# Performance work log

Measured on AMD Instinct MI355X. Metric: run time of the kernel, lower is better.

## Reference

```python
import jax, jax.numpy as jnp
import numpy as np

N, E, F, H, A, C, NC, L, AH = 50000, 800000, 768, 256, 128, 128, 7, 2, 4

def _ln(x, g, b):
    m = jnp.mean(x, axis=-1, keepdims=True)
    v = jnp.var(x, axis=-1, keepdims=True)
    return (x - m) / jnp.sqrt(v + 1e-5) * g + b

def setup_inputs() -> dict:
    key = jax.random.key(0)
    ks = jax.random.split(key, 32)
    s = 0.02
    d = {}
    d['x'] = jax.random.normal(ks[0], (N, F), jnp.float32)
    d['edge_index'] = jax.random.randint(ks[1], (2, E), 0, N, jnp.int32)
    d['W_in'] = jax.random.normal(ks[2], (F, H), jnp.float32) * s
    d['b_in'] = jnp.zeros((H,), jnp.float32)
    d['gin_W1'] = jax.random.normal(ks[3], (L, H, H), jnp.float32) * s
    d['gin_b1'] = jnp.zeros((L, H), jnp.float32)
    d['gin_lng'] = jnp.ones((L, H), jnp.float32)
    d['gin_lnb'] = jnp.zeros((L, H), jnp.float32)
    d['gin_W2'] = jax.random.normal(ks[4], (L, H, H), jnp.float32) * s
    d['gin_b2'] = jnp.zeros((L, H), jnp.float32)
    d['eps'] = jnp.zeros((L,), jnp.float32)
    d['ln_g'] = jnp.ones((L, H), jnp.float32)
    d['ln_b'] = jnp.zeros((L, H), jnp.float32)
    d['att_W1'] = jax.random.normal(ks[5], (AH, H, A), jnp.float32) * s
    d['att_b1'] = jnp.zeros((AH, A), jnp.float32)
    d['att_W2'] = jax.random.normal(ks[6], (AH, A), jnp.float32) * s
    d['att_b2'] = jnp.zeros((AH,), jnp.float32)
    d['Wc1'] = jax.random.normal(ks[7], (H, C), jnp.float32) * s
    d['bc1'] = jnp.zeros((C,), jnp.float32)
    d['lnc1_g'] = jnp.ones((C,), jnp.float32)
    d['lnc1_b'] = jnp.zeros((C,), jnp.float32)
    d['Wc2'] = jax.random.normal(ks[8], (C, C // 2), jnp.float32) * s
    d['bc2'] = jnp.zeros((C // 2,), jnp.float32)
    d['lnc2_g'] = jnp.ones((C // 2,), jnp.float32)
    d['lnc2_b'] = jnp.zeros((C // 2,), jnp.float32)
    d['Wc3'] = jax.random.normal(ks[9], (C // 2, NC), jnp.float32) * s
    d['bc3'] = jnp.zeros((NC,), jnp.float32)
    return d

def reference(x, edge_index, W_in, b_in, gin_W1, gin_b1, gin_lng, gin_lnb, gin_W2, gin_b2, eps, ln_g, ln_b, att_W1, att_b1, att_W2, att_b2, Wc1, bc1, lnc1_g, lnc1_b, Wc2, bc2, lnc2_g, lnc2_b, Wc3, bc3):
    src, dst = edge_index[0], edge_index[1]
    # input projection (use_residual and input_dim != gnn_hidden)
    h = x @ W_in + b_in  # [N,H]
    for i in range(L):
        agg = jax.ops.segment_sum(h[src], dst, num_segments=N)  # GIN sum aggregation
        m = (1.0 + eps[i]) * h + agg
        m = _ln(m @ gin_W1[i] + gin_b1[i], gin_lng[i], gin_lnb[i])
        m = jax.nn.relu(m) @ gin_W2[i] + gin_b2[i]
        hn = jax.nn.relu(_ln(m, ln_g[i], ln_b[i]))
        h = hn + h  # residual (shapes match)
    # multi-head attention pooling, softmax over node dim
    s = jnp.tanh(jnp.einsum('nd,kda->kna', h, att_W1) + att_b1[:, None, :])  # [AH,N,A]
    logits = jnp.einsum('kna,ka->kn', s, att_W2) + att_b2[:, None]  # [AH,N]
    a = jax.nn.softmax(logits, axis=1)  # [AH,N]
    z = jnp.einsum('kn,nd->kd', a, h)  # [AH,H]
    z_agg = jnp.mean(z, axis=0)  # [H]
    attn = a.T  # [N,AH]
    # classifier (full variant)
    c = jax.nn.relu(_ln(z_agg @ Wc1 + bc1, lnc1_g, lnc1_b))
    c = jax.nn.relu(_ln(c @ Wc2 + bc2, lnc2_g, lnc2_b))
    probs = jax.nn.softmax(c @ Wc3 + bc3, axis=0)
    return probs, attn
```

## Files before the change

### kernel.cpp

```cpp
#include <hip/hip_runtime.h>
#include <math.h>

#define NN 50000
#define NE 800000
#define FF 768
#define HH 256

typedef __attribute__((ext_vector_type(8))) short short8;
typedef __attribute__((ext_vector_type(4))) float f32x4;

__device__ inline unsigned short f2bf(float f) {
  unsigned u = __float_as_uint(f);
  u = u + 0x7fffu + ((u >> 16) & 1u);
  return (unsigned short)(u >> 16);
}
__device__ inline float bf2f(unsigned short b) {
  return __uint_as_float(((unsigned)b) << 16);
}

__device__ __forceinline__ void ldsload16(const unsigned short* g, unsigned short* l) {
  __builtin_amdgcn_global_load_lds(
      (const __attribute__((address_space(1))) void*)g,
      (__attribute__((address_space(3))) void*)l, 16, 0, 0);
}

__global__ void k_count(const int* __restrict__ dstv, int* __restrict__ deg) {
  int e = blockIdx.x * 256 + threadIdx.x;
  if (e < NE) atomicAdd(&deg[dstv[e]], 1);
}

__global__ void k_scan(const int* __restrict__ deg, int* __restrict__ rowptr) {
  const int CH = 49;
  int tid = threadIdx.x;
  int lane = tid & 63, w = tid >> 6;
  int base = tid * CH;
  int sum = 0;
  for (int i = 0; i < CH; i++) {
    int idx = base + i;
    if (idx < NN) sum += deg[idx];
  }
  int incl = sum;
  for (int off = 1; off < 64; off <<= 1) {
    int tv = __shfl_up(incl, off, 64);
    if (lane >= off) incl += tv;
  }
  __shared__ int ws[16];
  if (lane == 63) ws[w] = incl;
  __syncthreads();
  if (tid == 0) {
    int c = 0;
    for (int i = 0; i < 16; i++) { int tv = ws[i]; ws[i] = c; c += tv; }
  }
  __syncthreads();
  int run = ws[w] + (incl - sum);
  if (tid == 0) rowptr[0] = 0;
  for (int i = 0; i < CH; i++) {
    int idx = base + i;
    if (idx < NN) { run += deg[idx]; rowptr[idx + 1] = run; }
  }
}

__global__ void k_scatter(const int* __restrict__ srcv, const int* __restrict__ dstv,
                          int* __restrict__ cursor, int* __restrict__ csr_src) {
  int e = blockIdx.x * 256 + threadIdx.x;
  if (e < NE) {
    int d = dstv[e];
    int pos = atomicAdd(&cursor[d], 1);
    csr_src[pos] = srcv[e];
  }
}

__global__ void k_agg(const unsigned short* __restrict__ hb, const int* __restrict__ rowptr,
                      const int* __restrict__ csr_src, const float* __restrict__ eps,
                      int layer, unsigned short* __restrict__ mb) {
  int node = (blockIdx.x * blockDim.x + threadIdx.x) >> 6;
  int lane = threadIdx.x & 63;
  if (node >= NN) return;
  int beg = rowptr[node], end = rowptr[node + 1];
  const ushort4* hv = (const ushort4*)hb;
  float ax = 0.f, ay = 0.f, az = 0.f, aw = 0.f;
  for (int e = beg; e < end; ++e) {
    int s = csr_src[e];
    ushort4 v = hv[(size_t)s * 64 + lane];
    ax += bf2f(v.x); ay += bf2f(v.y); az += bf2f(v.z); aw += bf2f(v.w);
  }
  float ep = 1.0f + eps[layer];
  ushort4 h0 = hv[(size_t)node * 64 + lane];
  ax += ep * bf2f(h0.x); ay += ep * bf2f(h0.y);
  az += ep * bf2f(h0.z); aw += ep * bf2f(h0.w);
  ushort4 o;
  o.x = f2bf(ax); o.y = f2bf(ay); o.z = f2bf(az); o.w = f2bf(aw);
  *(ushort4*)&mb[(size_t)node * 256 + lane * 4] = o;
}

__global__ void k_tcast(const float* __restrict__ src0, unsigned short* __restrict__ dst0,
                        int R, int C) {
  const float* src = src0 + (size_t)blockIdx.z * R * C;
  unsigned short* dst = dst0 + (size_t)blockIdx.z * R * C;
  __shared__ float tile[32][33];
  int bx = blockIdx.x * 32, by = blockIdx.y * 32;
  int tx = threadIdx.x & 31, ty = threadIdx.x >> 5;
  for (int i = 0; i < 32; i += 8) {
    int r = by + ty + i, c = bx + tx;
    tile[ty + i][tx] = (r < R && c < C) ? src[(size_t)r * C + c] : 0.f;
  }
  __syncthreads();
  for (int i = 0; i < 32; i += 8) {
    int c = bx + ty + i, r = by + tx;
    if (c < C && r < R) dst[(size_t)c * R + r] = f2bf(tile[tx][ty + i]);
  }
}

template <int KTOT, int EPI, bool AF32, bool WF>
__global__ __launch_bounds__(256) void k_mm(
    const void* __restrict__ Ap, const unsigned short* __restrict__ Bt,
    const float* __restrict__ bias, const float* __restrict__ g,
    const float* __restrict__ be, const float* __restrict__ resid,
    float* __restrict__ outf, unsigned short* __restrict__ outb) {
  __shared__ unsigned short As[64 * 32];
  __shared__ unsigned short Bs[256 * 32];
  __shared__ float redS[4][64];
  __shared__ float redQ[4][64];
  __shared__ float mvM[64], mvI[64];
  int t = threadIdx.x, lane = t & 63, wave = t >> 6;
  int row0 = blockIdx.x * 64;
  f32x4 acc[4][4];
#pragma unroll
  for (int i = 0; i < 4; i++)
#pragma unroll
    for (int j = 0; j < 4; j++) acc[i][j] = (f32x4)(0.f);
  int m16 = lane & 15, kq = lane >> 4;

  int arow = t >> 2, a2 = t & 3;
  int asl = a2 ^ (arow & 3);
  int agr = row0 + arow; if (agr >= NN) agr = NN - 1;
  unsigned short* AsDst = &As[wave * 512];
  int brow_[4], bsl_[4];
#pragma unroll
  for (int j = 0; j < 4; j++) {
    int s = j * 256 + t;
    brow_[j] = s >> 2;
    bsl_[j] = (s & 3) ^ (brow_[j] & 3);
  }

  for (int k0 = 0; k0 < KTOT; k0 += 32) {
    if (AF32) {
      const float* Af = (const float*)Ap + (size_t)agr * KTOT + k0 + asl * 8;
      float4 f0 = *(const float4*)Af;
      float4 f1 = *(const float4*)(Af + 4);
      short8 v;
      v[0] = (short)f2bf(f0.x); v[1] = (short)f2bf(f0.y);
      v[2] = (short)f2bf(f0.z); v[3] = (short)f2bf(f0.w);
      v[4] = (short)f2bf(f1.x); v[5] = (short)f2bf(f1.y);
      v[6] = (short)f2bf(f1.z); v[7] = (short)f2bf(f1.w);
      *(short8*)&As[arow * 32 + a2 * 8] = v;
    } else {
      ldsload16((const unsigned short*)Ap + (size_t)agr * KTOT + k0 + asl * 8, AsDst);
    }
#pragma unroll
    for (int j = 0; j < 4; j++)
      ldsload16(&Bt[(size_t)brow_[j] * KTOT + k0 + bsl_[j] * 8],
                &Bs[(j * 256 + wave * 64) * 8]);
    __syncthreads();
    short8 a[4], b[4];
#pragma unroll
    for (int rt = 0; rt < 4; rt++) {
      int row = rt * 16 + m16;
      a[rt] = *(const short8*)&As[row * 32 + ((kq ^ (row & 3)) * 8)];
    }
#pragma unroll
    for (int ct = 0; ct < 4; ct++) {
      int row = wave * 64 + ct * 16 + m16;
      b[ct] = *(const short8*)&Bs[row * 32 + ((kq ^ (row & 3)) * 8)];
    }
#pragma unroll
    for (int rt = 0; rt < 4; rt++)
#pragma unroll
      for (int ct = 0; ct < 4; ct++)
        acc[rt][ct] = __builtin_amdgcn_mfma_f32_16x16x32_bf16(a[rt], b[ct], acc[rt][ct], 0, 0, 0);
    __syncthreads();
  }

  int colbase = wave * 64 + m16;
  float bv[4];
#pragma unroll
  for (int ct = 0; ct < 4; ct++) bv[ct] = bias[colbase + ct * 16];

  if (EPI == 0) {
#pragma unroll
    for (int rt = 0; rt < 4; rt++)
#pragma unroll
      for (int reg = 0; reg < 4; reg++) {
        int r = row0 + rt * 16 + kq * 4 + reg;
        if (r < NN) {
#pragma unroll
          for (int ct = 0; ct < 4; ct++) {
            float v = acc[rt][ct][reg] + bv[ct];
            outf[(size_t)r * 256 + colbase + ct * 16] = v;
            outb[(size_t)r * 256 + colbase + ct * 16] = f2bf(v);
          }
        }
      }
    return;
  }

  float s[4][4], q[4][4];
#pragma unroll
  for (int rt = 0; rt < 4; rt++)
#pragma unroll
    for (int reg = 0; reg < 4; reg++) { s[rt][reg] = 0.f; q[rt][reg] = 0.f; }
#pragma unroll
  for (int rt = 0; rt < 4; rt++)
#pragma unroll
    for (int ct = 0; ct < 4; ct++)
#pragma unroll
      for (int reg = 0; reg < 4; reg++) {
        float v = acc[rt][ct][reg] + bv[ct];
        acc[rt][ct][reg] = v;
        s[rt][reg] += v;
        q[rt][reg] += v * v;
      }
#pragma unroll
  for (int off = 1; off < 16; off <<= 1) {
#pragma unroll
    for (int rt = 0; rt < 4; rt++)
#pragma unroll
      for (int reg = 0; reg < 4; reg++) {
        s[rt][reg] += __shfl_xor(s[rt][reg], off, 64);
        q[rt][reg] += __shfl_xor(q[rt][reg], off, 64);
      }
  }
  if (m16 == 0) {
#pragma unroll
    for (int rt = 0; rt < 4; rt++)
#pragma unroll
      for (int reg = 0; reg < 4; reg++) {
        redS[wave][rt * 16 + kq * 4 + reg] = s[rt][reg];
        redQ[wave][rt * 16 + kq * 4 + reg] = q[rt][reg];
      }
  }
  __syncthreads();
  if (t < 64) {
    float ss = redS[0][t] + redS[1][t] + redS[2][t] + redS[3][t];
    float qq = redQ[0][t] + redQ[1][t] + redQ[2][t] + redQ[3][t];
    float mean = ss * (1.f / 256.f);
    float var = qq * (1.f / 256.f) - mean * mean;
    mvM[t] = mean;
    mvI[t] = rsqrtf(var + 1e-5f);
  }
  __syncthreads();
  float gv[4], bev[4];
#pragma unroll
  for (int ct = 0; ct < 4; ct++) { gv[ct] = g[colbase + ct * 16]; bev[ct] = be[colbase + ct * 16]; }
#pragma unroll
  for (int rt = 0; rt < 4; rt++)
#pragma unroll
    for (int reg = 0; reg < 4; reg++) {
      int rr = rt * 16 + kq * 4 + reg;
      int r = row0 + rr;
      if (r >= NN) continue;
      float mean = mvM[rr], inv = mvI[rr];
#pragma unroll
      for (int ct = 0; ct < 4; ct++) {
        int col = colbase + ct * 16;
        float val = fmaxf((acc[rt][ct][reg] - mean) * inv * gv[ct] + bev[ct], 0.f);
        if (EPI == 2) {
          val += resid[(size_t)r * 256 + col];
          if (WF) outf[(size_t)r * 256 + col] = val;
        }
        outb[(size_t)r * 256 + col] = f2bf(val);
      }
    }
}

__global__ __launch_bounds__(256) void k_att(const unsigned short* __restrict__ hb,
    const unsigned short* __restrict__ W1T, const float* __restrict__ b1,
    const float* __restrict__ W2, const float* __restrict__ b2,
    float* __restrict__ logitsT) {
  __shared__ unsigned short As[64 * 32];
  __shared__ unsigned short Bs[512 * 32];
  int t = threadIdx.x, lane = t & 63, wave = t >> 6;
  int row0 = blockIdx.x * 64;
  f32x4 acc[4][8];
#pragma unroll
  for (int i = 0; i < 4; i++)
#pragma unroll
    for (int j = 0; j < 8; j++) acc[i][j] = (f32x4)(0.f);
  int m16 = lane & 15, kq = lane >> 4;
  int arow = t >> 2, a2 = t & 3;
  int asl = a2 ^ (arow & 3);
  int agr = row0 + arow; if (agr >= NN) agr = NN - 1;
  unsigned short* AsDst = &As[wave * 512];
  int brow_[8], bsl_[8];
#pragma unroll
  for (int j = 0; j < 8; j++) {
    int s = j * 256 + t;
    brow_[j] = s >> 2;
    bsl_[j] = (s & 3) ^ (brow_[j] & 3);
  }
  for (int k0 = 0; k0 < 256; k0 += 32) {
    ldsload16(&hb[(size_t)agr * 256 + k0 + asl * 8], AsDst);
#pragma unroll
    for (int j = 0; j < 8; j++)
      ldsload16(&W1T[(size_t)brow_[j] * 256 + k0 + bsl_[j] * 8],
                &Bs[(j * 256 + wave * 64) * 8]);
    __syncthreads();
    short8 a[4];
#pragma unroll
    for (int rt = 0; rt < 4; rt++) {
      int row = rt * 16 + m16;
      a[rt] = *(const short8*)&As[row * 32 + ((kq ^ (row & 3)) * 8)];
    }
#pragma unroll
    for (int ct = 0; ct < 8; ct++) {
      int row = wave * 128 + ct * 16 + m16;
      short8 b = *(const short8*)&Bs[row * 32 + ((kq ^ (row & 3)) * 8)];
#pragma unroll
      for (int rt = 0; rt < 4; rt++)
        acc[rt][ct] = __builtin_amdgcn_mfma_f32_16x16x32_bf16(a[rt], b, acc[rt][ct], 0, 0, 0);
    }
    __syncthreads();
  }
  const float* b1k = b1 + wave * 128;
  const float* w2k = W2 + wave * 128;
  float p[4][4];
#pragma unroll
  for (int rt = 0; rt < 4; rt++)
#pragma unroll
    for (int reg = 0; reg < 4; reg++) p[rt][reg] = 0.f;
#pragma unroll
  for (int ct = 0; ct < 8; ct++) {
    int col = ct * 16 + m16;
    float b1v = b1k[col], w2v = w2k[col];
#pragma unroll
    for (int rt = 0; rt < 4; rt++)
#pragma unroll
      for (int reg = 0; reg < 4; reg++) {
        float xv = acc[rt][ct][reg] + b1v;
        xv = fminf(fmaxf(xv, -10.f), 10.f);
        float ex = __expf(2.f * xv);
        p[rt][reg] += (ex - 1.f) / (ex + 1.f) * w2v;
      }
  }
#pragma unroll
  for (int off = 1; off < 16; off <<= 1)
#pragma unroll
    for (int rt = 0; rt < 4; rt++)
#pragma unroll
      for (int reg = 0; reg < 4; reg++) p[rt][reg] += __shfl_xor(p[rt][reg], off, 64);
  if (m16 == 0) {
    float b2v = b2[wave];
#pragma unroll
    for (int rt = 0; rt < 4; rt++)
#pragma unroll
      for (int reg = 0; reg < 4; reg++) {
        int r = row0 + rt * 16 + kq * 4 + reg;
        if (r < NN) logitsT[(size_t)wave * NN + r] = p[rt][reg] + b2v;
      }
  }
}

__global__ void k_smax1(const float* __restrict__ logitsT, float* __restrict__ pmax,
                        float* __restrict__ psum) {
  int k = blockIdx.y;
  int tid = threadIdx.x;
  const float* L = logitsT + (size_t)k * NN;
  __shared__ float sm[256];
  float mx = -1e30f;
  for (int i = blockIdx.x * 256 + tid; i < NN; i += 128 * 256) mx = fmaxf(mx, L[i]);
  sm[tid] = mx; __syncthreads();
  for (int o = 128; o >= 1; o >>= 1) { if (tid < o) sm[tid] = fmaxf(sm[tid], sm[tid + o]); __syncthreads(); }
  float bmax = sm[0];
  __syncthreads();
  float s = 0.f;
  for (int i = blockIdx.x * 256 + tid; i < NN; i += 128 * 256) s += __expf(L[i] - bmax);
  sm[tid] = s; __syncthreads();
  for (int o = 128; o >= 1; o >>= 1) { if (tid < o) sm[tid] += sm[tid + o]; __syncthreads(); }
  if (tid == 0) { pmax[k * 128 + blockIdx.x] = bmax; psum[k * 128 + blockIdx.x] = sm[0]; }
}

__global__ void k_smax2(const float* __restrict__ pmax, const float* __restrict__ psum,
                        float* __restrict__ gs) {
  int k = blockIdx.x;
  int tid = threadIdx.x;
  __shared__ float sm[128], sv[128];
  float m = pmax[k * 128 + tid];
  sm[tid] = m; __syncthreads();
  for (int o = 64; o >= 1; o >>= 1) { if (tid < o) sm[tid] = fmaxf(sm[tid], sm[tid + o]); __syncthreads(); }
  float gm = sm[0];
  __syncthreads();
  sv[tid] = psum[k * 128 + tid] * __expf(m - gm);
  __syncthreads();
  for (int o = 64; o >= 1; o >>= 1) { if (tid < o) sv[tid] += sv[tid + o]; __syncthreads(); }
  if (tid == 0) { gs[k * 2] = gm; gs[k * 2 + 1] = sv[0]; }
}

__global__ void k_attnz(const float* __restrict__ logitsT, const float* __restrict__ gs,
                        const unsigned short* __restrict__ hb, float* __restrict__ out_attn,
                        float* __restrict__ z) {
  int n0 = blockIdx.x * 128;
  int tid = threadIdx.x;
  __shared__ float a[4][128];
  for (int i = tid; i < 512; i += 256) {
    int k = i >> 7, n = i & 127;
    float v = 0.f;
    if (n0 + n < NN) v = __expf(logitsT[(size_t)k * NN + n0 + n] - gs[k * 2]) / gs[k * 2 + 1];
    a[k][n] = v;
  }
  __syncthreads();
  for (int i = tid; i < 512; i += 256) {
    int n = i >> 2, k = i & 3;
    if (n0 + n < NN) out_attn[(size_t)(n0 + n) * 4 + k] = a[k][n];
  }
  float z0 = 0.f, z1 = 0.f, z2 = 0.f, z3 = 0.f;
  int d = tid;
  int nmax = NN - n0; if (nmax > 128) nmax = 128;
  for (int n = 0; n < nmax; n++) {
    float hv = bf2f(hb[(size_t)(n0 + n) * 256 + d]);
    z0 += a[0][n] * hv; z1 += a[1][n] * hv; z2 += a[2][n] * hv; z3 += a[3][n] * hv;
  }
  atomicAdd(&z[0 * 256 + d], z0);
  atomicAdd(&z[1 * 256 + d], z1);
  atomicAdd(&z[2 * 256 + d], z2);
  atomicAdd(&z[3 * 256 + d], z3);
}

__global__ void k_cls(const float* __restrict__ z, const float* __restrict__ Wc1,
                      const float* __restrict__ bc1, const float* __restrict__ g1,
                      const float* __restrict__ b1, const float* __restrict__ Wc2,
                      const float* __restrict__ bc2, const float* __restrict__ g2,
                      const float* __restrict__ b2, const float* __restrict__ Wc3,
                      const float* __restrict__ bc3, float* __restrict__ out) {
  int tid = threadIdx.x;
  __shared__ float za[256];
  __shared__ float buf[256];
  __shared__ float c1s[128];
  __shared__ float c2s[64];
  za[tid] = 0.25f * (z[tid] + z[256 + tid] + z[512 + tid] + z[768 + tid]);
  __syncthreads();
  float v1 = 0.f;
  if (tid < 128) {
    for (int d = 0; d < 256; d++) v1 += za[d] * Wc1[d * 128 + tid];
    v1 += bc1[tid];
  }
  buf[tid] = (tid < 128) ? v1 : 0.f; __syncthreads();
  for (int o = 128; o >= 1; o >>= 1) { if (tid < o) buf[tid] += buf[tid + o]; __syncthreads(); }
  float mean1 = buf[0] * (1.f / 128.f);
  __syncthreads();
  buf[tid] = (tid < 128) ? (v1 - mean1) * (v1 - mean1) : 0.f; __syncthreads();
  for (int o = 128; o >= 1; o >>= 1) { if (tid < o) buf[tid] += buf[tid + o]; __syncthreads(); }
  float inv1 = rsqrtf(buf[0] * (1.f / 128.f) + 1e-5f);
  __syncthreads();
  if (tid < 128) c1s[tid] = fmaxf((v1 - mean1) * inv1 * g1[tid] + b1[tid], 0.f);
  __syncthreads();
  float v2 = 0.f;
  if (tid < 64) {
    for (int d = 0; d < 128; d++) v2 += c1s[d] * Wc2[d * 64 + tid];
    v2 += bc2[tid];
  }
  buf[tid] = (tid < 64) ? v2 : 0.f; __syncthreads();
  for (int o = 128; o >= 1; o >>= 1) { if (tid < o) buf[tid] += buf[tid + o]; __syncthreads(); }
  float mean2 = buf[0] * (1.f / 64.f);
  __syncthreads();
  buf[tid] = (tid < 64) ? (v2 - mean2) * (v2 - mean2) : 0.f; __syncthreads();
  for (int o = 128; o >= 1; o >>= 1) { if (tid < o) buf[tid] += buf[tid + o]; __syncthreads(); }
  float inv2 = rsqrtf(buf[0] * (1.f / 64.f) + 1e-5f);
  __syncthreads();
  if (tid < 64) c2s[tid] = fmaxf((v2 - mean2) * inv2 * g2[tid] + b2[tid], 0.f);
  __syncthreads();
  if (tid < 7) {
    float l = 0.f;
    for (int d = 0; d < 64; d++) l += c2s[d] * Wc3[d * 7 + tid];
    buf[tid] = l + bc3[tid];
  }
  __syncthreads();
  if (tid == 0) {
    float mx = -1e30f;
    for (int i = 0; i < 7; i++) mx = fmaxf(mx, buf[i]);
    float s = 0.f;
    for (int i = 0; i < 7; i++) s += __expf(buf[i] - mx);
    for (int i = 0; i < 7; i++) out[i] = __expf(buf[i] - mx) / s;
  }
}

extern "C" void kernel_launch(void* const* d_in, const int* in_sizes, int n_in,
                              void* d_out, int out_size, void* d_ws, size_t ws_size,
                              hipStream_t stream) {
  const float* x       = (const float*)d_in[0];
  const int*   ei      = (const int*)d_in[1];
  const float* W_in    = (const float*)d_in[2];
  const float* b_in    = (const float*)d_in[3];
  const float* gin_W1  = (const float*)d_in[4];
  const float* gin_b1  = (const float*)d_in[5];
  const float* gin_lng = (const float*)d_in[6];
  const float* gin_lnb = (const float*)d_in[7];
  const float* gin_W2  = (const float*)d_in[8];
  const float* gin_b2  = (const float*)d_in[9];
  const float* eps     = (const float*)d_in[10];
  const float* ln_g    = (const float*)d_in[11];
  const float* ln_b    = (const float*)d_in[12];
  const float* att_W1  = (const float*)d_in[13];
  const float* att_b1  = (const float*)d_in[14];
  const float* att_W2  = (const float*)d_in[15];
  const float* att_b2  = (const float*)d_in[16];
  const float* Wc1     = (const float*)d_in[17];
  const float* bc1     = (const float*)d_in[18];
  const float* lnc1_g  = (const float*)d_in[19];
  const float* lnc1_b  = (const float*)d_in[20];
  const float* Wc2     = (const float*)d_in[21];
  const float* bc2     = (const float*)d_in[22];
  const float* lnc2_g  = (const float*)d_in[23];
  const float* lnc2_b  = (const float*)d_in[24];
  const float* Wc3     = (const float*)d_in[25];
  const float* bc3     = (const float*)d_in[26];
  float* out = (float*)d_out;
  (void)in_sizes; (void)n_in; (void)out_size; (void)ws_size;

  char* wsb = (char*)d_ws;
  size_t off = 0;
  auto alloc = [&](size_t bytes) {
    char* p = wsb + off;
    off += (bytes + 255) & ~(size_t)255;
    return p;
  };
  float*          h       = (float*)alloc((size_t)NN * HH * 4);
  unsigned short* hb      = (unsigned short*)alloc((size_t)NN * HH * 2);
  unsigned short* mb1     = (unsigned short*)alloc((size_t)NN * HH * 2);
  unsigned short* mb2     = (unsigned short*)alloc((size_t)NN * HH * 2);
  unsigned short* WinT    = (unsigned short*)alloc((size_t)HH * FF * 2);
  unsigned short* g1T     = (unsigned short*)alloc((size_t)2 * HH * HH * 2);
  unsigned short* g2T     = (unsigned short*)alloc((size_t)2 * HH * HH * 2);
  unsigned short* aW1T    = (unsigned short*)alloc((size_t)4 * 128 * HH * 2);
  float*          logitsT = (float*)alloc((size_t)4 * NN * 4);
  int*            deg     = (int*)alloc((size_t)NN * 4);
  int*            rowptr  = (int*)alloc((size_t)(NN + 1) * 4);
  int*            cursor  = (int*)alloc((size_t)NN * 4);
  int*            csr_src = (int*)alloc((size_t)NE * 4);
  float*          pmax    = (float*)alloc(4 * 128 * 4);
  float*          psum    = (float*)alloc(4 * 128 * 4);
  float*          gs      = (float*)alloc(8 * 4);
  float*          z       = (float*)alloc(4 * 256 * 4);

  const int* srcv = ei;
  const int* dstv = ei + NE;

  k_tcast<<<dim3((HH + 31) / 32, (FF + 31) / 32, 1), 256, 0, stream>>>(W_in, WinT, FF, HH);
  k_tcast<<<dim3(8, 8, 2), 256, 0, stream>>>(gin_W1, g1T, HH, HH);
  k_tcast<<<dim3(8, 8, 2), 256, 0, stream>>>(gin_W2, g2T, HH, HH);
  k_tcast<<<dim3(4, 8, 4), 256, 0, stream>>>(att_W1, aW1T, HH, 128);

  hipMemsetAsync(deg, 0, (size_t)NN * 4, stream);
  hipMemsetAsync(z, 0, 4 * 256 * 4, stream);
  k_count<<<(NE + 255) / 256, 256, 0, stream>>>(dstv, deg);
  k_scan<<<1, 1024, 0, stream>>>(deg, rowptr);
  hipMemcpyAsync(cursor, rowptr, (size_t)NN * 4, hipMemcpyDeviceToDevice, stream);
  k_scatter<<<(NE + 255) / 256, 256, 0, stream>>>(srcv, dstv, cursor, csr_src);

  int gblocks = (NN + 63) / 64;
  k_mm<FF, 0, true, true><<<gblocks, 256, 0, stream>>>(x, WinT, b_in, nullptr, nullptr, nullptr, h, hb);

  for (int l = 0; l < 2; l++) {
    k_agg<<<(NN + 3) / 4, 256, 0, stream>>>(hb, rowptr, csr_src, eps, l, mb1);
    k_mm<HH, 1, false, true><<<gblocks, 256, 0, stream>>>(mb1, g1T + (size_t)l * HH * HH,
        gin_b1 + l * HH, gin_lng + l * HH, gin_lnb + l * HH, nullptr, nullptr, mb2);
    if (l == 0)
      k_mm<HH, 2, false, true><<<gblocks, 256, 0, stream>>>(mb2, g2T + (size_t)l * HH * HH,
          gin_b2 + l * HH, ln_g + l * HH, ln_b + l * HH, h, h, hb);
    else
      k_mm<HH, 2, false, false><<<gblocks, 256, 0, stream>>>(mb2, g2T + (size_t)l * HH * HH,
          gin_b2 + l * HH, ln_g + l * HH, ln_b + l * HH, h, nullptr, hb);
  }

  k_att<<<gblocks, 256, 0, stream>>>(hb, aW1T, att_b1, att_W2, att_b2, logitsT);
  k_smax1<<<dim3(128, 4), 256, 0, stream>>>(logitsT, pmax, psum);
  k_smax2<<<4, 128, 0, stream>>>(pmax, psum, gs);
  k_attnz<<<(NN + 127) / 128, 256, 0, stream>>>(logitsT, gs, hb, out + 7, z);
  k_cls<<<1, 256, 0, stream>>>(z, Wc1, bc1, lnc1_g, lnc1_b, Wc2, bc2, lnc2_g, lnc2_b,
                               Wc3, bc3, out);
}
```

Baseline: 935.2 us.

## Double-buffer LDS loads in bf16 GIN matmuls with explicit waitcnt pipelining

Splits the templated matmul into a float-input projection kernel and a bf16-input hidden kernel. The hidden kernel double-buffers the A and B tiles in LDS, prefetching two K-chunks ahead with global_load_lds and using s_waitcnt vmcnt plus raw barriers so loads overlap the MFMA work. The goal is to hide global memory latency in the four 256-wide GIN matmuls. In exchange it doubles LDS use per block, which may lower occupancy, and it depends on hand-counted vmcnt values being correct.

```diff
diff --git a/kernel.cpp b/kernel.cpp
--- a/kernel.cpp
+++ b/kernel.cpp
@@ -111,17 +111,12 @@
   }
 }
 
-template <int KTOT, int EPI, bool AF32, bool WF>
-__global__ __launch_bounds__(256) void k_mm(
-    const void* __restrict__ Ap, const unsigned short* __restrict__ Bt,
-    const float* __restrict__ bias, const float* __restrict__ g,
-    const float* __restrict__ be, const float* __restrict__ resid,
-    float* __restrict__ outf, unsigned short* __restrict__ outb) {
+__global__ __launch_bounds__(256) void k_mmff(
+    const float* __restrict__ x, const unsigned short* __restrict__ Bt,
+    const float* __restrict__ bias, float* __restrict__ outf,
+    unsigned short* __restrict__ outb) {
   __shared__ unsigned short As[64 * 32];
   __shared__ unsigned short Bs[256 * 32];
-  __shared__ float redS[4][64];
-  __shared__ float redQ[4][64];
-  __shared__ float mvM[64], mvI[64];
   int t = threadIdx.x, lane = t & 63, wave = t >> 6;
   int row0 = blockIdx.x * 64;
   f32x4 acc[4][4];
@@ -130,11 +125,9 @@
 #pragma unroll
     for (int j = 0; j < 4; j++) acc[i][j] = (f32x4)(0.f);
   int m16 = lane & 15, kq = lane >> 4;
-
   int arow = t >> 2, a2 = t & 3;
   int asl = a2 ^ (arow & 3);
   int agr = row0 + arow; if (agr >= NN) agr = NN - 1;
-  unsigned short* AsDst = &As[wave * 512];
   int brow_[4], bsl_[4];
 #pragma unroll
   for (int j = 0; j < 4; j++) {
@@ -142,10 +135,9 @@
     brow_[j] = s >> 2;
     bsl_[j] = (s & 3) ^ (brow_[j] & 3);
   }
-
-  for (int k0 = 0; k0 < KTOT; k0 += 32) {
-    if (AF32) {
-      const float* Af = (const float*)Ap + (size_t)agr * KTOT + k0 + asl * 8;
+  for (int k0 = 0; k0 < FF; k0 += 32) {
+    {
+      const float* Af = x + (size_t)agr * FF + k0 + asl * 8;
       float4 f0 = *(const float4*)Af;
       float4 f1 = *(const float4*)(Af + 4);
       short8 v;
@@ -154,12 +146,10 @@
       v[4] = (short)f2bf(f1.x); v[5] = (short)f2bf(f1.y);
       v[6] = (short)f2bf(f1.z); v[7] = (short)f2bf(f1.w);
       *(short8*)&As[arow * 32 + a2 * 8] = v;
-    } else {
-      ldsload16((const unsigned short*)Ap + (size_t)agr * KTOT + k0 + asl * 8, AsDst);
     }
 #pragma unroll
     for (int j = 0; j < 4; j++)
-      ldsload16(&Bt[(size_t)brow_[j] * KTOT + k0 + bsl_[j] * 8],
+      ldsload16(&Bt[(size_t)brow_[j] * FF + k0 + bsl_[j] * 8],
                 &Bs[(j * 256 + wave * 64) * 8]);
     __syncthreads();
     short8 a[4], b[4];
@@ -180,29 +170,102 @@
         acc[rt][ct] = __builtin_amdgcn_mfma_f32_16x16x32_bf16(a[rt], b[ct], acc[rt][ct], 0, 0, 0);
     __syncthreads();
   }
-
   int colbase = wave * 64 + m16;
   float bv[4];
 #pragma unroll
   for (int ct = 0; ct < 4; ct++) bv[ct] = bias[colbase + ct * 16];
-
-  if (EPI == 0) {
-#pragma unroll
-    for (int rt = 0; rt < 4; rt++)
-#pragma unroll
-      for (int reg = 0; reg < 4; reg++) {
-        int r = row0 + rt * 16 + kq * 4 + reg;
-        if (r < NN) {
-#pragma unroll
-          for (int ct = 0; ct < 4; ct++) {
-            float v = acc[rt][ct][reg] + bv[ct];
-            outf[(size_t)r * 256 + colbase + ct * 16] = v;
-            outb[(size_t)r * 256 + colbase + ct * 16] = f2bf(v);
-          }
+#pragma unroll
+  for (int rt = 0; rt < 4; rt++)
+#pragma unroll
+    for (int reg = 0; reg < 4; reg++) {
+      int r = row0 + rt * 16 + kq * 4 + reg;
+      if (r < NN) {
+#pragma unroll
+        for (int ct = 0; ct < 4; ct++) {
+          float v = acc[rt][ct][reg] + bv[ct];
+          outf[(size_t)r * 256 + colbase + ct * 16] = v;
+          outb[(size_t)r * 256 + colbase + ct * 16] = f2bf(v);
         }
       }
-    return;
-  }
+    }
+}
+
+template <int EPI, bool WF>
+__global__ __launch_bounds__(256) void k_mmh(
+    const unsigned short* __restrict__ Ab, const unsigned short* __restrict__ Bt,
+    const float* __restrict__ bias, const float* __restrict__ g,
+    const float* __restrict__ be, const float* __restrict__ resid,
+    float* __restrict__ outf, unsigned short* __restrict__ outb) {
+  __shared__ unsigned short As[2][64 * 32];
+  __shared__ unsigned short Bs[2][256 * 32];
+  __shared__ float redS[4][64];
+  __shared__ float redQ[4][64];
+  __shared__ float mvM[64], mvI[64];
+  int t = threadIdx.x, lane = t & 63, wave = t >> 6;
+  int row0 = blockIdx.x * 64;
+  int m16 = lane & 15, kq = lane >> 4;
+  int arow = t >> 2, a2 = t & 3;
+  int asl = a2 ^ (arow & 3);
+  int agr = row0 + arow; if (agr >= NN) agr = NN - 1;
+  const unsigned short* Ag = Ab + (size_t)agr * 256 + asl * 8;
+  int brow_[4], bsl_[4];
+#pragma unroll
+  for (int j = 0; j < 4; j++) {
+    int s = j * 256 + t;
+    brow_[j] = s >> 2;
+    bsl_[j] = (s & 3) ^ (brow_[j] & 3);
+  }
+  auto stage = [&](int c, int p) {
+    int k0 = c * 32;
+    ldsload16(Ag + k0, &As[p][wave * 512]);
+#pragma unroll
+    for (int j = 0; j < 4; j++)
+      ldsload16(&Bt[(size_t)brow_[j] * 256 + k0 + bsl_[j] * 8],
+                &Bs[p][(j * 256 + wave * 64) * 8]);
+  };
+
+  f32x4 acc[4][4];
+#pragma unroll
+  for (int i = 0; i < 4; i++)
+#pragma unroll
+    for (int j = 0; j < 4; j++) acc[i][j] = (f32x4)(0.f);
+
+  stage(0, 0);
+  stage(1, 1);
+#pragma unroll
+  for (int c = 0; c < 8; c++) {
+    if (c < 7) asm volatile("s_waitcnt vmcnt(5)" ::: "memory");
+    else       asm volatile("s_waitcnt vmcnt(0)" ::: "memory");
+    __builtin_amdgcn_s_barrier();
+    asm volatile("" ::: "memory");
+    const unsigned short* Ap = As[c & 1];
+    const unsigned short* Bp = Bs[c & 1];
+    short8 a[4], b[4];
+#pragma unroll
+    for (int rt = 0; rt < 4; rt++) {
+      int row = rt * 16 + m16;
+      a[rt] = *(const short8*)&Ap[row * 32 + ((kq ^ (row & 3)) * 8)];
+    }
+#pragma unroll
+    for (int ct = 0; ct < 4; ct++) {
+      int row = wave * 64 + ct * 16 + m16;
+      b[ct] = *(const short8*)&Bp[row * 32 + ((kq ^ (row & 3)) * 8)];
+    }
+#pragma unroll
+    for (int rt = 0; rt < 4; rt++)
+#pragma unroll
+      for (int ct = 0; ct < 4; ct++)
+        acc[rt][ct] = __builtin_amdgcn_mfma_f32_16x16x32_bf16(a[rt], b[ct], acc[rt][ct], 0, 0, 0);
+    asm volatile("" ::: "memory");
+    __builtin_amdgcn_s_barrier();
+    asm volatile("" ::: "memory");
+    if (c + 2 < 8) stage(c + 2, c & 1);
+  }
+
+  int colbase = wave * 64 + m16;
+  float bv[4];
+#pragma unroll
+  for (int ct = 0; ct < 4; ct++) bv[ct] = bias[colbase + ct * 16];
 
   float s[4][4], q[4][4];
 #pragma unroll
@@ -557,17 +620,17 @@
   k_scatter<<<(NE + 255) / 256, 256, 0, stream>>>(srcv, dstv, cursor, csr_src);
 
   int gblocks = (NN + 63) / 64;
-  k_mm<FF, 0, true, true><<<gblocks, 256, 0, stream>>>(x, WinT, b_in, nullptr, nullptr, nullptr, h, hb);
+  k_mmff<<<gblocks, 256, 0, stream>>>(x, WinT, b_in, h, hb);
 
   for (int l = 0; l < 2; l++) {
     k_agg<<<(NN + 3) / 4, 256, 0, stream>>>(hb, rowptr, csr_src, eps, l, mb1);
-    k_mm<HH, 1, false, true><<<gblocks, 256, 0, stream>>>(mb1, g1T + (size_t)l * HH * HH,
+    k_mmh<1, true><<<gblocks, 256, 0, stream>>>(mb1, g1T + (size_t)l * HH * HH,
         gin_b1 + l * HH, gin_lng + l * HH, gin_lnb + l * HH, nullptr, nullptr, mb2);
     if (l == 0)
-      k_mm<HH, 2, false, true><<<gblocks, 256, 0, stream>>>(mb2, g2T + (size_t)l * HH * HH,
+      k_mmh<2, true><<<gblocks, 256, 0, stream>>>(mb2, g2T + (size_t)l * HH * HH,
           gin_b2 + l * HH, ln_g + l * HH, ln_b + l * HH, h, h, hb);
     else
-      k_mm<HH, 2, false, false><<<gblocks, 256, 0, stream>>>(mb2, g2T + (size_t)l * HH * HH,
+      k_mmh<2, false><<<gblocks, 256, 0, stream>>>(mb2, g2T + (size_t)l * HH * HH,
           gin_b2 + l * HH, ln_g + l * HH, ln_b + l * HH, h, nullptr, hb);
   }
 
```

Measured after the change: 931.4 us. No clear change (-0.4%).
